# Kernel tuning notes

Hardware: AMD Instinct MI355X
Metric: run time of the kernel (lower is better)

## Reference

```python
import jax, jax.numpy as jnp
import numpy as np

LAM = 0.5
MU = 0.1
RHO = 0.05


def setup_inputs() -> dict:
    key = jax.random.key(0)
    k1, k2, k3 = jax.random.split(key, 3)
    B, C, S = 65536, 10, 128
    predictions = jax.random.normal(k1, (B, C), dtype=jnp.float32)
    targets = jax.random.randint(k2, (B,), 0, C)
    noise = jax.random.normal(k3, (S, B, C), dtype=jnp.float32)
    return {"predictions": predictions, "targets": targets, "noise": noise}


def reference(predictions, targets, noise):
    B, C = predictions.shape
    # log-softmax of predictions, reused for all cross-entropies
    logp = jax.nn.log_softmax(predictions, axis=1)  # [B, C]
    # wstar = CE(predictions, hard targets), mean over batch
    wstar = -jnp.mean(jnp.take_along_axis(logp, targets[:, None], axis=1))
    one_hot = jax.nn.one_hot(targets, C, dtype=predictions.dtype)  # [B, C]
    # soft targets for each of the n_samples noise draws (vectorized over s)
    soft_lam = jax.nn.softmax(LAM * noise + one_hot, axis=-1)  # [S, B, C]
    soft = jax.nn.softmax(noise + one_hot, axis=-1)            # [S, B, C]
    # CE with soft (probability) targets: -mean_b sum_c target * log_softmax(pred)
    w = -jnp.einsum('sbc,bc->s', soft, logp) / B       # [S]
    wt = -jnp.einsum('sbc,bc->s', soft_lam, logp) / B  # [S]
    noise2 = jnp.sum(noise * noise, axis=(1, 2))       # [S]
    sc1 = jnp.maximum(wstar - wt, 0.0)
    sc2 = jnp.maximum(wstar - w + MU * noise2 / 2, 0.0)
    sc3 = jnp.maximum(wt - (1.0 - LAM) * wstar + LAM * w
                      + MU * LAM * (1.0 - LAM) * noise2 / 2, 0.0)
    sc = jnp.sum(sc1 + sc2 + sc3)  # aggregation='sum'
    return wstar + RHO * sc
```

## Files before the change

kernel.cpp:

```cpp
#include <hip/hip_runtime.h>

#define LAM 0.5f
#define MU 0.1f
#define RHO 0.05f
#define CLS 10
#define ROWS 256
#define SG 16
#define L2E  1.4426950408889634f
#define HL2E 0.7213475204444817f
#define EINV 0.36787944117144233f

typedef const __attribute__((address_space(1))) char gchar;
typedef __attribute__((address_space(3))) char lchar;

__device__ __forceinline__ float waveReduceSum(float v) {
#pragma unroll
    for (int m = 1; m < 64; m <<= 1) v += __shfl_xor(v, m, 64);
    return v;
}

__device__ __forceinline__ void dmaTile(const float4* srcBase, float* dstBase,
                                        int wid, int lane) {
    const float4* s = srcBase + wid * 160;
    float* d = dstBase + wid * 640;
    __builtin_amdgcn_global_load_lds((gchar*)(const char*)(s + lane),
                                     (lchar*)(char*)d, 16, 0, 0);
    __builtin_amdgcn_global_load_lds((gchar*)(const char*)(s + 64 + lane),
                                     (lchar*)(char*)(d + 256), 16, 0, 0);
    if (lane < 32)
        __builtin_amdgcn_global_load_lds((gchar*)(const char*)(s + 128 + lane),
                                         (lchar*)(char*)(d + 512), 16, 0, 0);
}

__global__ __launch_bounds__(256) void main_kernel(
    const float* __restrict__ noise, const float* __restrict__ pred,
    const int* __restrict__ tgt,
    float* __restrict__ wstarPart, float* __restrict__ partials, int B) {
    __shared__ float buf0[ROWS * CLS];
    __shared__ float buf1[ROWS * CLS];
    __shared__ float part[4][SG][3];
    __shared__ float red[4];
    const int tid = threadIdx.x;
    const int lane = tid & 63, wid = tid >> 6;
    const int nChunks = B / ROWS;
    const int chunk = blockIdx.x % nChunks;
    const int sg = blockIdx.x / nChunks;
    const int rowBase = chunk * ROWS;
    const int s0 = sg * SG;

    const int t = tgt[rowBase + tid];

    const float4* predT = (const float4*)(pred + (size_t)rowBase * CLS);
    const size_t sStride4 = (size_t)B * CLS / 4;
    const float4* noiseT = (const float4*)(noise + (size_t)rowBase * CLS)
                           + (size_t)s0 * sStride4;

    dmaTile(predT, buf0, wid, lane);
    dmaTile(noiseT, buf1, wid, lane);
    asm volatile("s_waitcnt vmcnt(3)" ::: "memory");
    __builtin_amdgcn_sched_barrier(0);

    float x[CLS];
    {
        const float2* r2 = (const float2*)(buf0 + tid * CLS);
#pragma unroll
        for (int j = 0; j < 5; j++) { float2 v = r2[j]; x[2*j] = v.x; x[2*j+1] = v.y; }
    }
    float mx = x[0];
#pragma unroll
    for (int c = 1; c < CLS; c++) mx = fmaxf(mx, x[c]);
    float z = 0.f;
#pragma unroll
    for (int c = 0; c < CLS; c++) z += __expf(x[c] - mx);
    float lse = mx + __logf(z);

    float lp[CLS], lpk[CLS], kk[CLS], bias[CLS];
    float xt = 0.f;
#pragma unroll
    for (int c = 0; c < CLS; c++) {
        bool e = (c == t);
        float lpv = x[c] - lse;
        lp[c] = lpv;
        kk[c] = e ? EINV : 1.f;
        lpk[c] = lpv * kk[c];
        bias[c] = e ? L2E : 0.f;
        xt += e ? x[c] : 0.f;
    }
    {
        float rce = waveReduceSum(lse - xt);
        if (lane == 0) red[wid] = rce;
    }

    const float4* srcNext = noiseT + sStride4;

#define BODY(CUR, NXT, SI)                                                     \
    {                                                                          \
        const int si = (SI);                                                   \
        if (si < SG - 1) {                                                     \
            dmaTile(srcNext, (NXT), wid, lane);                                \
            srcNext += sStride4;                                               \
            asm volatile("s_waitcnt vmcnt(3)" ::: "memory");                   \
        } else {                                                               \
            asm volatile("s_waitcnt vmcnt(0)" ::: "memory");                   \
        }                                                                      \
        __builtin_amdgcn_sched_barrier(0);                                     \
        float nn[CLS];                                                         \
        {                                                                      \
            const float2* r2 = (const float2*)((CUR) + tid * CLS);             \
            _Pragma("unroll")                                                  \
            for (int j = 0; j < 5; j++) {                                      \
                float2 v = r2[j]; nn[2*j] = v.x; nn[2*j+1] = v.y;              \
            }                                                                  \
        }                                                                      \
        float Z = 0.f, Zl = 0.f, dot = 0.f, dotl = 0.f, sq = 0.f;              \
        _Pragma("unroll")                                                      \
        for (int c = 0; c < CLS; c++) {                                        \
            float a  = fmaf(nn[c], HL2E, bias[c]);                             \
            float pl = exp2f(a);                                               \
            float t1 = pl * pl;                                                \
            Zl += pl;                                                          \
            dotl = fmaf(pl, lp[c], dotl);                                      \
            Z    = fmaf(t1, kk[c], Z);                                         \
            dot  = fmaf(t1, lpk[c], dot);                                      \
            sq   = fmaf(nn[c], nn[c], sq);                                     \
        }                                                                      \
        float rw  = waveReduceSum(__fdividef(dot, Z));                         \
        float rwt = waveReduceSum(__fdividef(dotl, Zl));                       \
        float rn2 = waveReduceSum(sq);                                         \
        if (lane == 0) {                                                       \
            part[wid][si][0] = rw;                                             \
            part[wid][si][1] = rwt;                                            \
            part[wid][si][2] = rn2;                                            \
        }                                                                      \
    }

    for (int sb = 0; sb < SG; sb += 2) {
        BODY(buf1, buf0, sb);
        BODY(buf0, buf1, sb + 1);
    }
#undef BODY

    __syncthreads();
    if (tid < SG * 3) {
        int si = tid / 3, ki = tid % 3;
        float v = part[0][si][ki] + part[1][si][ki] + part[2][si][ki] + part[3][si][ki];
        partials[((size_t)(s0 + si) * 3 + ki) * nChunks + chunk] = v;
    }
    if (sg == 0 && tid == 0)
        wstarPart[chunk] = red[0] + red[1] + red[2] + red[3];
}

__global__ __launch_bounds__(1024) void tail_kernel(
    const float* __restrict__ partials, const float* __restrict__ wstarPart,
    float* __restrict__ out, int B, int S, int nChunks) {
    __shared__ float sres[3 * 128];
    __shared__ float wred[4];
    __shared__ float scred[2];
    const int tid = threadIdx.x;
    const int lane = tid & 63, wid = tid >> 6;
    const int nRows = 3 * S;

    for (int r = wid; r < nRows; r += 16) {
        const float* row = partials + (size_t)r * nChunks;
        float v = 0.f;
#pragma unroll 4
        for (int j = lane; j < nChunks; j += 64) v += row[j];
        v = waveReduceSum(v);
        if (lane == 0) sres[r] = v;
    }

    if (tid < 256) {
        float v = (tid < nChunks) ? wstarPart[tid] : 0.f;
        v = waveReduceSum(v);
        if (lane == 0) wred[wid] = v;
    }
    __syncthreads();

    float invB = 1.0f / (float)B;
    float wstar = (wred[0] + wred[1] + wred[2] + wred[3]) * invB;
    float local = 0.f;
    if (tid < S) {
        float w  = -sres[3 * tid + 0] * invB;
        float wt = -sres[3 * tid + 1] * invB;
        float n2 =  sres[3 * tid + 2];
        float sc1 = fmaxf(wstar - wt, 0.f);
        float sc2 = fmaxf(wstar - w + MU * n2 * 0.5f, 0.f);
        float sc3 = fmaxf(wt - (1.f - LAM) * wstar + LAM * w
                          + MU * LAM * (1.f - LAM) * n2 * 0.5f, 0.f);
        local = sc1 + sc2 + sc3;
    }
    if (tid < 128) {
        float rsc = waveReduceSum(local);
        if (lane == 0) scred[wid] = rsc;
    }
    __syncthreads();
    if (tid == 0) out[0] = wstar + RHO * (scred[0] + scred[1]);
}

extern "C" void kernel_launch(void* const* d_in, const int* in_sizes, int n_in,
                              void* d_out, int out_size, void* d_ws, size_t ws_size,
                              hipStream_t stream) {
    const float* pred  = (const float*)d_in[0];
    const int*   tgt   = (const int*)d_in[1];
    const float* noise = (const float*)d_in[2];
    float* out = (float*)d_out;

    int B = in_sizes[1];
    int S = in_sizes[2] / in_sizes[0];
    int nChunks = B / ROWS;
    int nSG = S / SG;

    float* ws = (float*)d_ws;
    float* wstarPart = ws;
    float* partials  = ws + nChunks;

    main_kernel<<<nSG * nChunks, 256, 0, stream>>>(noise, pred, tgt,
                                                   wstarPart, partials, B);
    tail_kernel<<<1, 1024, 0, stream>>>(partials, wstarPart, out, B, S, nChunks);
}
```

Baseline: 84.76 us.

## Fuse tail reduction into main kernel with atomic counters and deeper DMA pipeline

```diff
diff --git a/kernel.cpp b/kernel.cpp
--- a/kernel.cpp
+++ b/kernel.cpp
@@ -5,10 +5,12 @@
 #define RHO 0.05f
 #define CLS 10
 #define ROWS 256
-#define SG 16
+#define SG 64
+#define DEPTH 3
 #define L2E  1.4426950408889634f
 #define HL2E 0.7213475204444817f
 #define EINV 0.36787944117144233f
+#define AGENT __HIP_MEMORY_SCOPE_AGENT
 
 typedef const __attribute__((address_space(1))) char gchar;
 typedef __attribute__((address_space(3))) char lchar;
@@ -32,37 +34,47 @@
                                          (lchar*)(char*)(d + 512), 16, 0, 0);
 }
 
-__global__ __launch_bounds__(256) void main_kernel(
+__global__ __launch_bounds__(256) void fused_kernel(
     const float* __restrict__ noise, const float* __restrict__ pred,
-    const int* __restrict__ tgt,
-    float* __restrict__ wstarPart, float* __restrict__ partials, int B) {
-    __shared__ float buf0[ROWS * CLS];
-    __shared__ float buf1[ROWS * CLS];
-    __shared__ float part[4][SG][3];
+    const int* __restrict__ tgt, float* __restrict__ ws,
+    float* __restrict__ out, int B, int S) {
+    __shared__ float4 buf4[4 * 640];
+    __shared__ float part[4 * SG * 3];
     __shared__ float red[4];
+    __shared__ float scred[2];
+    __shared__ unsigned flagA, flagB;
+    float* buf = (float*)buf4;
+
     const int tid = threadIdx.x;
     const int lane = tid & 63, wid = tid >> 6;
     const int nChunks = B / ROWS;
-    const int chunk = blockIdx.x % nChunks;
-    const int sg = blockIdx.x / nChunks;
+    const int chunk = (int)blockIdx.x % nChunks;
+    const int g = (int)blockIdx.x / nChunks;
     const int rowBase = chunk * ROWS;
-    const int s0 = sg * SG;
+    const int s0 = g * SG;
+
+    float* wstarPart = ws;
+    float* sres2     = ws + 256;
+    unsigned* cnts   = (unsigned*)(ws + 6400);
+    float* partials  = ws + 8192;
 
     const int t = tgt[rowBase + tid];
-
-    const float4* predT = (const float4*)(pred + (size_t)rowBase * CLS);
+    __builtin_amdgcn_sched_barrier(0);
+
     const size_t sStride4 = (size_t)B * CLS / 4;
     const float4* noiseT = (const float4*)(noise + (size_t)rowBase * CLS)
                            + (size_t)s0 * sStride4;
 
-    dmaTile(predT, buf0, wid, lane);
-    dmaTile(noiseT, buf1, wid, lane);
-    asm volatile("s_waitcnt vmcnt(3)" ::: "memory");
+    dmaTile((const float4*)(pred + (size_t)rowBase * CLS), buf + 3 * 2560, wid, lane);
+    dmaTile(noiseT,                buf,            wid, lane);
+    dmaTile(noiseT + sStride4,     buf + 2560,     wid, lane);
+    dmaTile(noiseT + 2 * sStride4, buf + 2 * 2560, wid, lane);
+    asm volatile("s_waitcnt vmcnt(9)" ::: "memory");
     __builtin_amdgcn_sched_barrier(0);
 
     float x[CLS];
     {
-        const float2* r2 = (const float2*)(buf0 + tid * CLS);
+        const float2* r2 = (const float2*)(buf + 3 * 2560 + tid * CLS);
 #pragma unroll
         for (int j = 0; j < 5; j++) { float2 v = r2[j]; x[2*j] = v.x; x[2*j+1] = v.y; }
     }
@@ -91,26 +103,14 @@
         if (lane == 0) red[wid] = rce;
     }
 
-    const float4* srcNext = noiseT + sStride4;
-
-#define BODY(CUR, NXT, SI)                                                     \
+#define COMPUTE(IT)                                                            \
     {                                                                          \
-        const int si = (SI);                                                   \
-        if (si < SG - 1) {                                                     \
-            dmaTile(srcNext, (NXT), wid, lane);                                \
-            srcNext += sStride4;                                               \
-            asm volatile("s_waitcnt vmcnt(3)" ::: "memory");                   \
-        } else {                                                               \
-            asm volatile("s_waitcnt vmcnt(0)" ::: "memory");                   \
-        }                                                                      \
-        __builtin_amdgcn_sched_barrier(0);                                     \
+        const int itv = (IT);                                                  \
+        const float2* r2 = (const float2*)(buf + (itv & 3) * 2560 + tid * CLS);\
         float nn[CLS];                                                         \
-        {                                                                      \
-            const float2* r2 = (const float2*)((CUR) + tid * CLS);             \
-            _Pragma("unroll")                                                  \
-            for (int j = 0; j < 5; j++) {                                      \
-                float2 v = r2[j]; nn[2*j] = v.x; nn[2*j+1] = v.y;              \
-            }                                                                  \
+        _Pragma("unroll")                                                      \
+        for (int j = 0; j < 5; j++) {                                          \
+            float2 v = r2[j]; nn[2*j] = v.x; nn[2*j+1] = v.y;                  \
         }                                                                      \
         float Z = 0.f, Zl = 0.f, dot = 0.f, dotl = 0.f, sq = 0.f;              \
         _Pragma("unroll")                                                      \
@@ -128,73 +128,103 @@
         float rwt = waveReduceSum(__fdividef(dotl, Zl));                       \
         float rn2 = waveReduceSum(sq);                                         \
         if (lane == 0) {                                                       \
-            part[wid][si][0] = rw;                                             \
-            part[wid][si][1] = rwt;                                            \
-            part[wid][si][2] = rn2;                                            \
+            part[wid * 192 + itv * 3 + 0] = rw;                                \
+            part[wid * 192 + itv * 3 + 1] = rwt;                               \
+            part[wid * 192 + itv * 3 + 2] = rn2;                               \
         }                                                                      \
     }
 
-    for (int sb = 0; sb < SG; sb += 2) {
-        BODY(buf1, buf0, sb);
-        BODY(buf0, buf1, sb + 1);
-    }
-#undef BODY
+    const float4* srcNext = noiseT + DEPTH * sStride4;
+    int it = 0;
+#pragma unroll 1
+    for (; it < SG - DEPTH; ++it) {
+        asm volatile("s_waitcnt vmcnt(6)" ::: "memory");
+        __builtin_amdgcn_sched_barrier(0);
+        dmaTile(srcNext, buf + ((it + DEPTH) & 3) * 2560, wid, lane);
+        srcNext += sStride4;
+        COMPUTE(it);
+    }
+    asm volatile("s_waitcnt vmcnt(0)" ::: "memory");
+    __builtin_amdgcn_sched_barrier(0);
+#pragma unroll 1
+    for (; it < SG; ++it) COMPUTE(it);
+#undef COMPUTE
 
     __syncthreads();
     if (tid < SG * 3) {
-        int si = tid / 3, ki = tid % 3;
-        float v = part[0][si][ki] + part[1][si][ki] + part[2][si][ki] + part[3][si][ki];
-        partials[((size_t)(s0 + si) * 3 + ki) * nChunks + chunk] = v;
-    }
-    if (sg == 0 && tid == 0)
-        wstarPart[chunk] = red[0] + red[1] + red[2] + red[3];
-}
-
-__global__ __launch_bounds__(1024) void tail_kernel(
-    const float* __restrict__ partials, const float* __restrict__ wstarPart,
-    float* __restrict__ out, int B, int S, int nChunks) {
-    __shared__ float sres[3 * 128];
-    __shared__ float wred[4];
-    __shared__ float scred[2];
-    const int tid = threadIdx.x;
-    const int lane = tid & 63, wid = tid >> 6;
-    const int nRows = 3 * S;
-
-    for (int r = wid; r < nRows; r += 16) {
-        const float* row = partials + (size_t)r * nChunks;
-        float v = 0.f;
+        float v = part[tid] + part[192 + tid] + part[384 + tid] + part[576 + tid];
+        __hip_atomic_store(&partials[(size_t)chunk * 384 + g * 192 + tid], v,
+                           __ATOMIC_RELAXED, AGENT);
+    }
+    if (g == 0 && tid == 255)
+        __hip_atomic_store(&wstarPart[chunk], red[0] + red[1] + red[2] + red[3],
+                           __ATOMIC_RELAXED, AGENT);
+    __syncthreads();
+
+    const int cg = chunk >> 4;
+    if (tid == 0) {
+        __threadfence();
+        unsigned old = __hip_atomic_fetch_add(&cnts[cg * 32], 1u,
+                                              __ATOMIC_ACQ_REL, AGENT);
+        flagA = ((old & 31u) == 31u);
+    }
+    __syncthreads();
+    if (flagA) {
+        float acc0 = 0.f, acc1 = 0.f;
+        const float* pbase = partials + (size_t)(cg * 16) * 384;
 #pragma unroll 4
-        for (int j = lane; j < nChunks; j += 64) v += row[j];
-        v = waveReduceSum(v);
-        if (lane == 0) sres[r] = v;
-    }
-
-    if (tid < 256) {
-        float v = (tid < nChunks) ? wstarPart[tid] : 0.f;
-        v = waveReduceSum(v);
-        if (lane == 0) wred[wid] = v;
-    }
-    __syncthreads();
-
-    float invB = 1.0f / (float)B;
-    float wstar = (wred[0] + wred[1] + wred[2] + wred[3]) * invB;
-    float local = 0.f;
-    if (tid < S) {
-        float w  = -sres[3 * tid + 0] * invB;
-        float wt = -sres[3 * tid + 1] * invB;
-        float n2 =  sres[3 * tid + 2];
-        float sc1 = fmaxf(wstar - wt, 0.f);
-        float sc2 = fmaxf(wstar - w + MU * n2 * 0.5f, 0.f);
-        float sc3 = fmaxf(wt - (1.f - LAM) * wstar + LAM * w
-                          + MU * LAM * (1.f - LAM) * n2 * 0.5f, 0.f);
-        local = sc1 + sc2 + sc3;
-    }
-    if (tid < 128) {
-        float rsc = waveReduceSum(local);
-        if (lane == 0) scred[wid] = rsc;
-    }
-    __syncthreads();
-    if (tid == 0) out[0] = wstar + RHO * (scred[0] + scred[1]);
+        for (int c = 0; c < 16; ++c) {
+            acc0 += __hip_atomic_load(&pbase[c * 384 + tid], __ATOMIC_RELAXED, AGENT);
+            if (tid < 128)
+                acc1 += __hip_atomic_load(&pbase[c * 384 + 256 + tid], __ATOMIC_RELAXED, AGENT);
+        }
+        __hip_atomic_store(&sres2[(size_t)tid * 16 + cg], acc0, __ATOMIC_RELAXED, AGENT);
+        if (tid < 128)
+            __hip_atomic_store(&sres2[(size_t)(256 + tid) * 16 + cg], acc1,
+                               __ATOMIC_RELAXED, AGENT);
+        __syncthreads();
+        if (tid == 0) {
+            __threadfence();
+            unsigned old2 = __hip_atomic_fetch_add(&cnts[16 * 32], 1u,
+                                                   __ATOMIC_ACQ_REL, AGENT);
+            flagB = ((old2 & 15u) == 15u);
+        }
+        __syncthreads();
+        if (flagB) {
+            float* sresL = part;
+            for (int r = tid; r < 384; r += 256) {
+                float v = 0.f;
+#pragma unroll
+                for (int q = 0; q < 16; ++q)
+                    v += __hip_atomic_load(&sres2[(size_t)r * 16 + q],
+                                           __ATOMIC_RELAXED, AGENT);
+                sresL[r] = v;
+            }
+            float wv = __hip_atomic_load(&wstarPart[tid], __ATOMIC_RELAXED, AGENT);
+            wv = waveReduceSum(wv);
+            if (lane == 0) red[wid] = wv;
+            __syncthreads();
+            float invB = 1.0f / (float)B;
+            float wstar = (red[0] + red[1] + red[2] + red[3]) * invB;
+            float local = 0.f;
+            if (tid < S) {
+                float w  = -sresL[3 * tid + 0] * invB;
+                float wt = -sresL[3 * tid + 1] * invB;
+                float n2 =  sresL[3 * tid + 2];
+                float sc1 = fmaxf(wstar - wt, 0.f);
+                float sc2 = fmaxf(wstar - w + MU * n2 * 0.5f, 0.f);
+                float sc3 = fmaxf(wt - (1.f - LAM) * wstar + LAM * w
+                                  + MU * LAM * (1.f - LAM) * n2 * 0.5f, 0.f);
+                local = sc1 + sc2 + sc3;
+            }
+            if (tid < 128) {
+                float rsc = waveReduceSum(local);
+                if (lane == 0) scred[wid] = rsc;
+            }
+            __syncthreads();
+            if (tid == 0) out[0] = wstar + RHO * (scred[0] + scred[1]);
+        }
+    }
 }
 
 extern "C" void kernel_launch(void* const* d_in, const int* in_sizes, int n_in,
@@ -210,11 +240,8 @@
     int nChunks = B / ROWS;
     int nSG = S / SG;
 
-    float* ws = (float*)d_ws;
-    float* wstarPart = ws;
-    float* partials  = ws + nChunks;
-
-    main_kernel<<<nSG * nChunks, 256, 0, stream>>>(noise, pred, tgt,
-                                                   wstarPart, partials, B);
-    tail_kernel<<<1, 1024, 0, stream>>>(partials, wstarPart, out, B, S, nChunks);
-}
+    hipMemsetAsync((char*)d_ws + 25600, 0, 2560, stream);
+
+    fused_kernel<<<nSG * nChunks, 256, 0, stream>>>(noise, pred, tgt,
+                                                    (float*)d_ws, out, B, S);
+}
```

Result: slower. 136.5 us (+61.0%).

## Drop LDS partial staging and parallelize final reduction across per-sample blocks

Applied to the files above, without the earlier changes.

```diff
diff --git a/kernel.cpp b/kernel.cpp
--- a/kernel.cpp
+++ b/kernel.cpp
@@ -38,24 +38,24 @@
     float* __restrict__ wstarPart, float* __restrict__ partials, int B) {
     __shared__ float buf0[ROWS * CLS];
     __shared__ float buf1[ROWS * CLS];
-    __shared__ float part[4][SG][3];
-    __shared__ float red[4];
+
     const int tid = threadIdx.x;
     const int lane = tid & 63, wid = tid >> 6;
     const int nChunks = B / ROWS;
-    const int chunk = blockIdx.x % nChunks;
-    const int sg = blockIdx.x / nChunks;
+    const int chunk = (int)blockIdx.x % nChunks;
+    const int sg = (int)blockIdx.x / nChunks;
     const int rowBase = chunk * ROWS;
     const int s0 = sg * SG;
+    const int nPart = nChunks * 4;
 
     const int t = tgt[rowBase + tid];
-
-    const float4* predT = (const float4*)(pred + (size_t)rowBase * CLS);
+    __builtin_amdgcn_sched_barrier(0);
+
     const size_t sStride4 = (size_t)B * CLS / 4;
     const float4* noiseT = (const float4*)(noise + (size_t)rowBase * CLS)
                            + (size_t)s0 * sStride4;
 
-    dmaTile(predT, buf0, wid, lane);
+    dmaTile((const float4*)(pred + (size_t)rowBase * CLS), buf0, wid, lane);
     dmaTile(noiseT, buf1, wid, lane);
     asm volatile("s_waitcnt vmcnt(3)" ::: "memory");
     __builtin_amdgcn_sched_barrier(0);
@@ -86,9 +86,10 @@
         bias[c] = e ? L2E : 0.f;
         xt += e ? x[c] : 0.f;
     }
+    float keep;
     {
         float rce = waveReduceSum(lse - xt);
-        if (lane == 0) red[wid] = rce;
+        keep = (lane == 48) ? rce : 0.f;
     }
 
     const float4* srcNext = noiseT + sStride4;
@@ -127,11 +128,9 @@
         float rw  = waveReduceSum(__fdividef(dot, Z));                         \
         float rwt = waveReduceSum(__fdividef(dotl, Zl));                       \
         float rn2 = waveReduceSum(sq);                                         \
-        if (lane == 0) {                                                       \
-            part[wid][si][0] = rw;                                             \
-            part[wid][si][1] = rwt;                                            \
-            part[wid][si][2] = rn2;                                            \
-        }                                                                      \
+        keep = (lane == si * 3    ) ? rw  : keep;                              \
+        keep = (lane == si * 3 + 1) ? rwt : keep;                              \
+        keep = (lane == si * 3 + 2) ? rn2 : keep;                              \
     }
 
     for (int sb = 0; sb < SG; sb += 2) {
@@ -140,61 +139,64 @@
     }
 #undef BODY
 
+    if (lane < SG * 3) {
+        int si = lane / 3, k = lane - 3 * si;
+        partials[(size_t)((s0 + si) * 3 + k) * nPart + chunk * 4 + wid] = keep;
+    }
+    if (sg == 0 && lane == 48)
+        wstarPart[chunk * 4 + wid] = keep;
+}
+
+__global__ __launch_bounds__(256) void reduce_kernel(
+    const float* __restrict__ partials, const float* __restrict__ wstarPart,
+    float* __restrict__ scPart, float* __restrict__ wsum, int B, int nPart) {
+    __shared__ float red[4][4];
+    const int s = blockIdx.x, tid = threadIdx.x;
+    const int lane = tid & 63, wid = tid >> 6;
+    const float* p = partials + (size_t)s * 3 * nPart;
+    float a = 0.f, b = 0.f, c = 0.f, wv = 0.f;
+    for (int j = tid; j < nPart; j += 256) {
+        a  += p[j];
+        b  += p[nPart + j];
+        c  += p[2 * nPart + j];
+        wv += wstarPart[j];
+    }
+    a = waveReduceSum(a); b = waveReduceSum(b);
+    c = waveReduceSum(c); wv = waveReduceSum(wv);
+    if (lane == 0) { red[wid][0] = a; red[wid][1] = b; red[wid][2] = c; red[wid][3] = wv; }
     __syncthreads();
-    if (tid < SG * 3) {
-        int si = tid / 3, ki = tid % 3;
-        float v = part[0][si][ki] + part[1][si][ki] + part[2][si][ki] + part[3][si][ki];
-        partials[((size_t)(s0 + si) * 3 + ki) * nChunks + chunk] = v;
-    }
-    if (sg == 0 && tid == 0)
-        wstarPart[chunk] = red[0] + red[1] + red[2] + red[3];
-}
-
-__global__ __launch_bounds__(1024) void tail_kernel(
-    const float* __restrict__ partials, const float* __restrict__ wstarPart,
-    float* __restrict__ out, int B, int S, int nChunks) {
-    __shared__ float sres[3 * 128];
-    __shared__ float wred[4];
-    __shared__ float scred[2];
-    const int tid = threadIdx.x;
-    const int lane = tid & 63, wid = tid >> 6;
-    const int nRows = 3 * S;
-
-    for (int r = wid; r < nRows; r += 16) {
-        const float* row = partials + (size_t)r * nChunks;
-        float v = 0.f;
-#pragma unroll 4
-        for (int j = lane; j < nChunks; j += 64) v += row[j];
-        v = waveReduceSum(v);
-        if (lane == 0) sres[r] = v;
-    }
-
-    if (tid < 256) {
-        float v = (tid < nChunks) ? wstarPart[tid] : 0.f;
-        v = waveReduceSum(v);
-        if (lane == 0) wred[wid] = v;
-    }
-    __syncthreads();
-
-    float invB = 1.0f / (float)B;
-    float wstar = (wred[0] + wred[1] + wred[2] + wred[3]) * invB;
-    float local = 0.f;
-    if (tid < S) {
-        float w  = -sres[3 * tid + 0] * invB;
-        float wt = -sres[3 * tid + 1] * invB;
-        float n2 =  sres[3 * tid + 2];
+    if (tid == 0) {
+        float ra = red[0][0] + red[1][0] + red[2][0] + red[3][0];
+        float rb = red[0][1] + red[1][1] + red[2][1] + red[3][1];
+        float rc = red[0][2] + red[1][2] + red[2][2] + red[3][2];
+        float rw = red[0][3] + red[1][3] + red[2][3] + red[3][3];
+        float invB = 1.0f / (float)B;
+        float wstar = rw * invB;
+        float w  = -ra * invB;
+        float wt = -rb * invB;
+        float n2 =  rc;
         float sc1 = fmaxf(wstar - wt, 0.f);
         float sc2 = fmaxf(wstar - w + MU * n2 * 0.5f, 0.f);
         float sc3 = fmaxf(wt - (1.f - LAM) * wstar + LAM * w
                           + MU * LAM * (1.f - LAM) * n2 * 0.5f, 0.f);
-        local = sc1 + sc2 + sc3;
-    }
+        scPart[s] = sc1 + sc2 + sc3;
+        if (s == 0) wsum[0] = rw;
+    }
+}
+
+__global__ __launch_bounds__(256) void finalize_kernel(
+    const float* __restrict__ scPart, const float* __restrict__ wsum,
+    float* __restrict__ out, int B, int S) {
+    __shared__ float red[2];
+    const int tid = threadIdx.x, lane = tid & 63, wid = tid >> 6;
+    float v = (tid < S) ? scPart[tid] : 0.f;
     if (tid < 128) {
-        float rsc = waveReduceSum(local);
-        if (lane == 0) scred[wid] = rsc;
+        float r = waveReduceSum(v);
+        if (lane == 0) red[wid] = r;
     }
     __syncthreads();
-    if (tid == 0) out[0] = wstar + RHO * (scred[0] + scred[1]);
+    if (tid == 0)
+        out[0] = wsum[0] / (float)B + RHO * (red[0] + red[1]);
 }
 
 extern "C" void kernel_launch(void* const* d_in, const int* in_sizes, int n_in,
@@ -209,12 +211,17 @@
     int S = in_sizes[2] / in_sizes[0];
     int nChunks = B / ROWS;
     int nSG = S / SG;
+    int nPart = nChunks * 4;
 
     float* ws = (float*)d_ws;
     float* wstarPart = ws;
-    float* partials  = ws + nChunks;
+    float* scPart    = ws + 1024;
+    float* wsum      = ws + 1152;
+    float* partials  = ws + 2048;
 
     main_kernel<<<nSG * nChunks, 256, 0, stream>>>(noise, pred, tgt,
                                                    wstarPart, partials, B);
-    tail_kernel<<<1, 1024, 0, stream>>>(partials, wstarPart, out, B, S, nChunks);
-}
+    reduce_kernel<<<S, 256, 0, stream>>>(partials, wstarPart, scPart, wsum,
+                                         B, nPart);
+    finalize_kernel<<<1, 256, 0, stream>>>(scPart, wsum, out, B, S);
+}
```

After: 74.20 us. -12.5%, faster.
